# Optimization experiments

Hardware: AMD Instinct MI355X
Metric: run time of the kernel (lower is better)

The kernel has to match this reference:

```python
import jax, jax.numpy as jnp
import numpy as np

T_NO = 200
COS_NO = 24
HID_NO = 10


def make_cos_basis(t_no=T_NO, n=COS_NO, scale=6.0, shift=1.0):
    # [n, t_no] raised-cosine log-time basis, matching the torch loop
    phi = (jnp.pi / 2.0) * jnp.arange(n, dtype=jnp.float32)[:, None]
    x = jnp.arange(t_no, dtype=jnp.float32)[None, :]
    raw = scale * jnp.log(x + shift + 1e-7)
    b = 0.5 * jnp.cos(raw - phi) + 0.5
    keep = (raw >= phi - jnp.pi) & (raw <= phi + jnp.pi)
    return jnp.where(keep, b, 0.0)


def causal_basis_conv(syn, basis):
    # syn: [B, sub, T]; basis: [K, T_no]
    # out[b,s,k,t] = sum_d basis[k,d] * syn[b,s,t-d]   (causal conv)
    B, sub, T = syn.shape
    K, t_no = basis.shape
    w = jnp.flip(basis, axis=1)                    # cross-corr of flipped = conv
    kern = jnp.tile(w, (sub, 1))[:, None, :]       # [sub*K, 1, T_no]
    out = jax.lax.conv_general_dilated(
        syn, kern, window_strides=(1,), padding=[(t_no - 1, 0)],
        feature_group_count=sub,
        dimension_numbers=("NCH", "OIH", "NCH"))   # [B, sub*K, T]
    return out.reshape(B, sub, K, T)


def reference(S_e, S_i, temp, test, g_e, g_i, E_scale, I_scale,
              W_e_layer1, W_i_layer1, W_layer2, b_layer1,
              C_syn_e_raw, C_syn_i_raw, V_o):
    sub_no = C_syn_e_raw.shape[0]
    batch, T_data, _ = S_e.shape

    if test:  # inference branch (near-hard assignment via huge temperature)
        C_syn_e = jax.nn.softmax(C_syn_e_raw * 10000.0, axis=0)
        C_syn_i = jax.nn.softmax(C_syn_i_raw * 10000.0, axis=0)
    else:     # CustomSoftmax.forward == softmax(x * 1000, dim=0)
        C_syn_e = jax.nn.softmax((C_syn_e_raw + g_e) * 1000.0, axis=0)
        C_syn_i = jax.nn.softmax((C_syn_i_raw + g_i) * 1000.0, axis=0)

    # per-synapse scaling then synapse -> subunit grouping
    syn_e = jnp.einsum('bte,se->bst', S_e * jnp.exp(E_scale)[None, None, :], C_syn_e)
    syn_i = jnp.einsum('bti,si->bst', S_i * jnp.exp(I_scale)[None, None, :], C_syn_i)

    basis = make_cos_basis()                         # [24, T_no]
    Be = causal_basis_conv(syn_e, basis)             # [B, sub, 24, T]
    Bi = causal_basis_conv(syn_i, basis)

    We = W_e_layer1.reshape(sub_no, HID_NO, COS_NO)
    Wi = W_i_layer1.reshape(sub_no, HID_NO, COS_NO)
    # linear combination over basis == original per-channel kernels (linearity)
    pre = (jnp.einsum('bskt,shk->bsht', Be, We)
           + jnp.einsum('bskt,shk->bsht', Bi, Wi)
           + b_layer1.reshape(1, sub_no, HID_NO, 1))
    layer1_out = jnp.tanh(pre)                       # [B, sub, hid, T]

    # grouped 1x1 conv with exp(W_layer2): weighted sum over hid per subunit
    sub_out = jnp.einsum('bsht,sh->bts', layer1_out, jnp.exp(W_layer2))  # [B, T, sub]
    final = jnp.sum(sub_out, -1) + V_o               # [B, T]
    return (final, sub_out, C_syn_e, C_syn_i)


def setup_inputs() -> dict:
    key = jax.random.key(0)
    ks = jax.random.split(key, 8)
    batch, T_data = 4, 20000
    sub_no, E_no, I_no = 20, 2000, 500
    return {
        "S_e": jax.random.uniform(ks[0], (batch, T_data, E_no), jnp.float32),
        "S_i": jax.random.uniform(ks[1], (batch, T_data, I_no), jnp.float32),
        "temp": 1,
        "test": 1,
        "g_e": jax.random.normal(ks[2], (sub_no, E_no), jnp.float32),
        "g_i": jax.random.normal(ks[3], (sub_no, I_no), jnp.float32),
        "E_scale": jnp.zeros((E_no,), jnp.float32),
        "I_scale": jnp.zeros((I_no,), jnp.float32),
        "W_e_layer1": jax.random.normal(ks[4], (sub_no * HID_NO, COS_NO), jnp.float32) * 0.01,
        "W_i_layer1": jax.random.normal(ks[5], (sub_no * HID_NO, COS_NO), jnp.float32) * 0.01,
        "W_layer2": jnp.ones((sub_no, HID_NO), jnp.float32) * -1.0,
        "b_layer1": jnp.zeros((sub_no * HID_NO,), jnp.float32),
        "C_syn_e_raw": jax.random.normal(ks[6], (sub_no, E_no), jnp.float32) * 0.01,
        "C_syn_i_raw": jax.random.normal(ks[7], (sub_no, I_no), jnp.float32) * 0.01,
        "V_o": jnp.zeros((1,), jnp.float32),
    }
```

## Files before the change

### kernel.cpp

```cpp
#include <hip/hip_runtime.h>
#include <math.h>

#define B_   4
#define T_   20000
#define SUB  20
#define ENO  2000
#define INO  500
#define HID  10
#define NCOS 24
#define TNO  200

__global__ __launch_bounds__(256) void prep1_kernel(
    const float* __restrict__ Ce_raw, const float* __restrict__ Ci_raw,
    const float* __restrict__ ge, const float* __restrict__ gi,
    const float* __restrict__ Es, const float* __restrict__ Is,
    const float* __restrict__ W2, const int* __restrict__ testp,
    float* __restrict__ outCe, float* __restrict__ outCi,
    float* __restrict__ CwE, float* __restrict__ CwI, float* __restrict__ e2)
{
  int idx = blockIdx.x * 256 + threadIdx.x;
  int test = *testp;
  float scale = test ? 10000.f : 1000.f;
  if (idx < ENO + INO) {
    const float* raw; const float* g; float* outC; float* Cw; int n, col; float sc;
    if (idx < ENO) { raw = Ce_raw; g = ge; outC = outCe; Cw = CwE; n = ENO; col = idx;      sc = expf(Es[col]); }
    else           { raw = Ci_raw; g = gi; outC = outCi; Cw = CwI; n = INO; col = idx - ENO; sc = expf(Is[col]); }
    float v[SUB]; float m = -1e30f;
    #pragma unroll
    for (int s = 0; s < SUB; s++) {
      float x = raw[s * n + col];
      if (!test) x += g[s * n + col];
      x *= scale;
      v[s] = x; m = fmaxf(m, x);
    }
    float sum = 0.f;
    #pragma unroll
    for (int s = 0; s < SUB; s++) { v[s] = expf(v[s] - m); sum += v[s]; }
    float inv = 1.f / sum;
    #pragma unroll
    for (int s = 0; s < SUB; s++) { float c = v[s] * inv; outC[s * n + col] = c; Cw[s * n + col] = c * sc; }
  } else if (idx < ENO + INO + SUB * HID) {
    int j = idx - (ENO + INO);
    e2[j] = expf(W2[j]);
  }
}

__global__ __launch_bounds__(256) void prep2_kernel(
    const float* __restrict__ We, const float* __restrict__ Wi, float* __restrict__ Keff)
{
  int idx = blockIdx.x * 256 + threadIdx.x;
  if (idx >= 2 * SUB * HID * TNO) return;
  int d   = idx % TNO;
  int sh  = (idx / TNO) % (SUB * HID);
  int src = idx / (TNO * SUB * HID);
  const float* W = src ? Wi : We;
  const float PIF = 3.14159265358979323846f;
  float raw = 6.0f * logf((float)d + 1.0f + 1e-7f);
  float acc = 0.f;
  #pragma unroll
  for (int k = 0; k < NCOS; k++) {
    float ph = 1.57079632679489662f * (float)k;
    if (raw >= ph - PIF && raw <= ph + PIF) {
      acc += W[sh * NCOS + k] * (0.5f * cosf(raw - ph) + 0.5f);
    }
  }
  Keff[idx] = acc;
}

__global__ __launch_bounds__(256, 2) void gemm_syn_kernel(
    const float* __restrict__ S_e, const float* __restrict__ S_i,
    const float* __restrict__ CwE, const float* __restrict__ CwI,
    float* __restrict__ synE, float* __restrict__ synI)
{
  const int b  = blockIdx.y;
  const int t0 = blockIdx.x * 16;

  __shared__ __align__(16) float sS[16 * 528];
  __shared__ __align__(16) float sCw[20 * 512];

  const int tid = threadIdx.x;
  const int l   = tid & 63;
  const int w   = tid >> 6;
  const int s0  = w * 5;
  const int tg  = l & 1;
  const int ep  = l >> 1;

  if (tid < 192)            { int r = tid / 12, c = tid % 12;            sS[r * 528 + 500 + c] = 0.f; }
  else if (tid < 432)       { int u = tid - 192; int s = u / 12, c = u % 12; sCw[s * 512 + 500 + c] = 0.f; }

  float acc[8][5] = {};

  for (int z = 0; z < 5; z++) {
    const bool isE = (z < 4);
    {
      const float* __restrict__ src = isE ? (S_e + ((long)(b * T_ + t0)) * ENO + z * 500)
                                          : (S_i + ((long)(b * T_ + t0)) * INO);
      const int rs = isE ? ENO : INO;
      for (int u = tid; u < 2000; u += 256) {
        int r = u / 125, k = u - r * 125;
        float4 v = *(const float4*)&src[(long)r * rs + 4 * k];
        *(float4*)&sS[r * 528 + 4 * k] = v;
      }
      const float* __restrict__ csrc = isE ? (CwE + z * 500) : CwI;
      const int cs2 = isE ? ENO : INO;
      for (int u = tid; u < 2500; u += 256) {
        int s = u / 125, k = u - s * 125;
        float4 v = *(const float4*)&csrc[(long)s * cs2 + 4 * k];
        *(float4*)&sCw[s * 512 + 4 * k] = v;
      }
    }
    __syncthreads();

    #pragma unroll
    for (int step = 0; step < 4; step++) {
      const int e = 4 * ep + 128 * step;
      float4 cw[5];
      #pragma unroll
      for (int j = 0; j < 5; j++) cw[j] = *(float4*)&sCw[(s0 + j) * 512 + e];
      #pragma unroll
      for (int tt = 0; tt < 8; tt++) {
        float4 sv = *(float4*)&sS[(tg + 2 * tt) * 528 + e];
        #pragma unroll
        for (int j = 0; j < 5; j++) {
          acc[tt][j] += sv.x * cw[j].x;
          acc[tt][j] += sv.y * cw[j].y;
          acc[tt][j] += sv.z * cw[j].z;
          acc[tt][j] += sv.w * cw[j].w;
        }
      }
    }
    __syncthreads();

    if (z == 3 || z == 4) {
      #pragma unroll
      for (int mask = 2; mask <= 32; mask <<= 1) {
        #pragma unroll
        for (int tt = 0; tt < 8; tt++)
          #pragma unroll
          for (int j = 0; j < 5; j++)
            acc[tt][j] += __shfl_xor(acc[tt][j], mask, 64);
      }
      float* __restrict__ dst = (z == 3) ? synE : synI;
      if (l < 2) {
        #pragma unroll
        for (int j = 0; j < 5; j++)
          #pragma unroll
          for (int tt = 0; tt < 8; tt++)
            dst[((long)b * SUB + s0 + j) * T_ + t0 + tg + 2 * tt] = acc[tt][j];
      }
      #pragma unroll
      for (int tt = 0; tt < 8; tt++)
        #pragma unroll
        for (int j = 0; j < 5; j++) acc[tt][j] = 0.f;
    }
  }
}

__global__ __launch_bounds__(256, 2) void conv_kernel(
    const float* __restrict__ synE, const float* __restrict__ synI,
    const float* __restrict__ Keff, const float* __restrict__ e2,
    const float* __restrict__ b1, float* __restrict__ sub_bst)
{
  const int chunk = blockIdx.x;
  const int s = blockIdx.y;
  const int b = blockIdx.z;
  const int cs = chunk * 1000;

  __shared__ __align__(16) float se[1200];
  __shared__ __align__(16) float si[1200];
  __shared__ __align__(16) float te[HID * TNO];
  __shared__ __align__(16) float ti[HID * TNO];
  __shared__ float se2[HID], sb[HID];

  const int tid = threadIdx.x;
  const float* __restrict__ pe = &synE[((long)b * SUB + s) * T_];
  const float* __restrict__ pin = &synI[((long)b * SUB + s) * T_];

  for (int i4 = tid; i4 < 300; i4 += 256) {
    int gt = cs - 200 + i4 * 4;
    float4 ve = make_float4(0.f, 0.f, 0.f, 0.f);
    float4 vi = make_float4(0.f, 0.f, 0.f, 0.f);
    if (gt >= 0) { ve = *(const float4*)&pe[gt]; vi = *(const float4*)&pin[gt]; }
    *(float4*)&se[i4 * 4] = ve;
    *(float4*)&si[i4 * 4] = vi;
  }
  const float* __restrict__ ke = &Keff[(long)s * HID * TNO];
  const float* __restrict__ ki = &Keff[((long)SUB + s) * HID * TNO];
  for (int i4 = tid; i4 < 500; i4 += 256) {
    *(float4*)&te[i4 * 4] = *(const float4*)&ke[i4 * 4];
    *(float4*)&ti[i4 * 4] = *(const float4*)&ki[i4 * 4];
  }
  if (tid < HID) { se2[tid] = e2[s * HID + tid]; sb[tid] = b1[s * HID + tid]; }
  __syncthreads();

  if (tid >= 250) return;
  const int lofs = 200 + 4 * tid;
  float so[4] = {0.f, 0.f, 0.f, 0.f};

  #pragma unroll
  for (int half = 0; half < 2; half++) {
    const int h0 = half * 5;
    float acc[5][4] = {};
    float we[8], wi[8];
    *(float4*)&we[4] = *(float4*)&se[lofs];
    *(float4*)&wi[4] = *(float4*)&si[lofs];
    for (int dstep = 0; dstep < 50; dstep++) {
      const int d0 = dstep * 4;
      *(float4*)&we[0] = *(float4*)&se[lofs - d0 - 4];
      *(float4*)&wi[0] = *(float4*)&si[lofs - d0 - 4];
      float4 tpe[5], tpi[5];
      #pragma unroll
      for (int h = 0; h < 5; h++) {
        tpe[h] = *(float4*)&te[(h0 + h) * TNO + d0];
        tpi[h] = *(float4*)&ti[(h0 + h) * TNO + d0];
      }
      #pragma unroll
      for (int dd = 0; dd < 4; dd++) {
        #pragma unroll
        for (int h = 0; h < 5; h++) {
          float tapeh = ((float*)&tpe[h])[dd];
          float tapih = ((float*)&tpi[h])[dd];
          #pragma unroll
          for (int j = 0; j < 4; j++) {
            acc[h][j] += tapeh * we[4 + j - dd];
            acc[h][j] += tapih * wi[4 + j - dd];
          }
        }
      }
      #pragma unroll
      for (int m = 0; m < 4; m++) { we[4 + m] = we[m]; wi[4 + m] = wi[m]; }
    }
    #pragma unroll
    for (int h = 0; h < 5; h++) {
      float eh = se2[h0 + h], bh = sb[h0 + h];
      #pragma unroll
      for (int j = 0; j < 4; j++) so[j] += eh * tanhf(acc[h][j] + bh);
    }
  }
  int t0 = cs + 4 * tid;
  *(float4*)&sub_bst[((long)b * SUB + s) * T_ + t0] = *(float4*)&so[0];
}

__global__ __launch_bounds__(256) void final_kernel(
    const float* __restrict__ sub_bst, const float* __restrict__ Vo,
    float* __restrict__ out_final, float* __restrict__ out_sub)
{
  int t = blockIdx.x * 256 + threadIdx.x;
  int b = blockIdx.y;
  if (t >= T_) return;
  float vo = Vo[0];
  float sum = 0.f;
  #pragma unroll
  for (int s = 0; s < SUB; s++) {
    float v = sub_bst[((long)b * SUB + s) * T_ + t];
    sum += v;
    out_sub[(((long)b * T_) + t) * SUB + s] = v;
  }
  out_final[(long)b * T_ + t] = sum + vo;
}

extern "C" void kernel_launch(void* const* d_in, const int* in_sizes, int n_in,
                              void* d_out, int out_size, void* d_ws, size_t ws_size,
                              hipStream_t stream)
{
  const float* S_e    = (const float*)d_in[0];
  const float* S_i    = (const float*)d_in[1];
  const int*   testp  = (const int*)d_in[3];
  const float* g_e    = (const float*)d_in[4];
  const float* g_i    = (const float*)d_in[5];
  const float* Es     = (const float*)d_in[6];
  const float* Is     = (const float*)d_in[7];
  const float* We     = (const float*)d_in[8];
  const float* Wi     = (const float*)d_in[9];
  const float* W2     = (const float*)d_in[10];
  const float* b1     = (const float*)d_in[11];
  const float* Ce_raw = (const float*)d_in[12];
  const float* Ci_raw = (const float*)d_in[13];
  const float* Vo     = (const float*)d_in[14];

  float* ws   = (float*)d_ws;
  float* CwE  = ws;
  float* CwI  = ws + 40000;
  float* Keff = ws + 50000;
  float* e2   = ws + 130000;
  float* synE = ws + 130200;
  float* synI = synE + 1600000;
  float* subb = synI + 1600000;

  float* out     = (float*)d_out;
  float* o_final = out;
  float* o_sub   = out + 80000;
  float* o_Ce    = out + 1680000;
  float* o_Ci    = out + 1720000;

  prep1_kernel<<<11, 256, 0, stream>>>(Ce_raw, Ci_raw, g_e, g_i, Es, Is, W2, testp,
                                       o_Ce, o_Ci, CwE, CwI, e2);
  prep2_kernel<<<(2 * SUB * HID * TNO + 255) / 256, 256, 0, stream>>>(We, Wi, Keff);
  gemm_syn_kernel<<<dim3(T_ / 16, B_), 256, 0, stream>>>(S_e, S_i, CwE, CwI, synE, synI);
  conv_kernel<<<dim3(20, SUB, B_), 256, 0, stream>>>(synE, synI, Keff, e2, b1, subb);
  final_kernel<<<dim3((T_ + 255) / 256, B_), 256, 0, stream>>>(subb, Vo, o_final, o_sub);
}
```

Before: 740.0 us.

## Prefetch S tiles into registers and read padded Cw weights from global

```diff
diff --git a/kernel.cpp b/kernel.cpp
--- a/kernel.cpp
+++ b/kernel.cpp
@@ -16,15 +16,15 @@
     const float* __restrict__ Es, const float* __restrict__ Is,
     const float* __restrict__ W2, const int* __restrict__ testp,
     float* __restrict__ outCe, float* __restrict__ outCi,
-    float* __restrict__ CwE, float* __restrict__ CwI, float* __restrict__ e2)
+    float* __restrict__ CwPE, float* __restrict__ CwPI, float* __restrict__ e2)
 {
   int idx = blockIdx.x * 256 + threadIdx.x;
   int test = *testp;
   float scale = test ? 10000.f : 1000.f;
   if (idx < ENO + INO) {
-    const float* raw; const float* g; float* outC; float* Cw; int n, col; float sc;
-    if (idx < ENO) { raw = Ce_raw; g = ge; outC = outCe; Cw = CwE; n = ENO; col = idx;      sc = expf(Es[col]); }
-    else           { raw = Ci_raw; g = gi; outC = outCi; Cw = CwI; n = INO; col = idx - ENO; sc = expf(Is[col]); }
+    const float* raw; const float* g; float* outC; int n, col; float sc;
+    if (idx < ENO) { raw = Ce_raw; g = ge; outC = outCe; n = ENO; col = idx;       sc = expf(Es[col]); }
+    else           { raw = Ci_raw; g = gi; outC = outCi; n = INO; col = idx - ENO; sc = expf(Is[col]); }
     float v[SUB]; float m = -1e30f;
     #pragma unroll
     for (int s = 0; s < SUB; s++) {
@@ -37,11 +37,27 @@
     #pragma unroll
     for (int s = 0; s < SUB; s++) { v[s] = expf(v[s] - m); sum += v[s]; }
     float inv = 1.f / sum;
-    #pragma unroll
-    for (int s = 0; s < SUB; s++) { float c = v[s] * inv; outC[s * n + col] = c; Cw[s * n + col] = c * sc; }
+    if (idx < ENO) {
+      int z = col / 500, e2c = col - z * 500;
+      #pragma unroll
+      for (int s = 0; s < SUB; s++) {
+        float c = v[s] * inv; outC[s * n + col] = c;
+        CwPE[((long)(z * SUB + s)) * 512 + e2c] = c * sc;
+      }
+    } else {
+      #pragma unroll
+      for (int s = 0; s < SUB; s++) {
+        float c = v[s] * inv; outC[s * n + col] = c;
+        CwPI[(long)s * 512 + col] = c * sc;
+      }
+    }
   } else if (idx < ENO + INO + SUB * HID) {
     int j = idx - (ENO + INO);
     e2[j] = expf(W2[j]);
+  } else if (idx < ENO + INO + SUB * HID + 960 + 240) {
+    int j = idx - (ENO + INO + SUB * HID);
+    if (j < 960) { int z = j / 240, s = (j / 12) % SUB, c = j % 12; CwPE[((long)(z * SUB + s)) * 512 + 500 + c] = 0.f; }
+    else         { int j2 = j - 960; int s = j2 / 12, c = j2 % 12;  CwPI[(long)s * 512 + 500 + c] = 0.f; }
   }
 }
 
@@ -67,59 +83,65 @@
   Keff[idx] = acc;
 }
 
-__global__ __launch_bounds__(256, 2) void gemm_syn_kernel(
+__global__ __launch_bounds__(256, 4) void gemm_syn_kernel(
     const float* __restrict__ S_e, const float* __restrict__ S_i,
-    const float* __restrict__ CwE, const float* __restrict__ CwI,
+    const float* __restrict__ CwPE, const float* __restrict__ CwPI,
     float* __restrict__ synE, float* __restrict__ synI)
 {
   const int b  = blockIdx.y;
   const int t0 = blockIdx.x * 16;
-
   __shared__ __align__(16) float sS[16 * 528];
-  __shared__ __align__(16) float sCw[20 * 512];
 
   const int tid = threadIdx.x;
   const int l   = tid & 63;
   const int w   = tid >> 6;
   const int s0  = w * 5;
-  const int tg  = l & 1;
-  const int ep  = l >> 1;
-
-  if (tid < 192)            { int r = tid / 12, c = tid % 12;            sS[r * 528 + 500 + c] = 0.f; }
-  else if (tid < 432)       { int u = tid - 192; int s = u / 12, c = u % 12; sCw[s * 512 + 500 + c] = 0.f; }
-
-  float acc[8][5] = {};
+  const int rp  = l & 3;
+  const int ep  = l >> 2;
+
+  if (tid < 192) { int r = tid / 12, c = tid % 12; sS[r * 528 + 500 + c] = 0.f; }
+
+  float acc[4][5] = {};
+  float4 pS[8];
+
+  const long rowE = ((long)b * T_ + t0) * ENO;
+  const long rowI = ((long)b * T_ + t0) * INO;
+
+  #pragma unroll
+  for (int p = 0; p < 8; p++) {
+    int u = tid + 256 * p;
+    if (u < 2000) { int r = u / 125, k = u - r * 125; pS[p] = *(const float4*)&S_e[rowE + (long)r * ENO + 4 * k]; }
+  }
 
   for (int z = 0; z < 5; z++) {
     const bool isE = (z < 4);
-    {
-      const float* __restrict__ src = isE ? (S_e + ((long)(b * T_ + t0)) * ENO + z * 500)
-                                          : (S_i + ((long)(b * T_ + t0)) * INO);
-      const int rs = isE ? ENO : INO;
-      for (int u = tid; u < 2000; u += 256) {
-        int r = u / 125, k = u - r * 125;
-        float4 v = *(const float4*)&src[(long)r * rs + 4 * k];
-        *(float4*)&sS[r * 528 + 4 * k] = v;
-      }
-      const float* __restrict__ csrc = isE ? (CwE + z * 500) : CwI;
-      const int cs2 = isE ? ENO : INO;
-      for (int u = tid; u < 2500; u += 256) {
-        int s = u / 125, k = u - s * 125;
-        float4 v = *(const float4*)&csrc[(long)s * cs2 + 4 * k];
-        *(float4*)&sCw[s * 512 + 4 * k] = v;
+    #pragma unroll
+    for (int p = 0; p < 8; p++) {
+      int u = tid + 256 * p;
+      if (u < 2000) { int r = u / 125, k = u - r * 125; *(float4*)&sS[r * 528 + 4 * k] = pS[p]; }
+    }
+    if (z < 4) {
+      const bool nE = (z + 1 < 4);
+      const float* __restrict__ src = nE ? (S_e + rowE + (z + 1) * 500) : (S_i + rowI);
+      const int rs = nE ? ENO : INO;
+      #pragma unroll
+      for (int p = 0; p < 8; p++) {
+        int u = tid + 256 * p;
+        if (u < 2000) { int r = u / 125, k = u - r * 125; pS[p] = *(const float4*)&src[(long)r * rs + 4 * k]; }
       }
     }
     __syncthreads();
 
-    #pragma unroll
-    for (int step = 0; step < 4; step++) {
-      const int e = 4 * ep + 128 * step;
+    const float* __restrict__ cwb = isE ? (CwPE + ((long)z * SUB) * 512) : CwPI;
+    #pragma unroll
+    for (int step = 0; step < 8; step++) {
+      const int e = 4 * ep + 64 * step;
       float4 cw[5];
       #pragma unroll
-      for (int j = 0; j < 5; j++) cw[j] = *(float4*)&sCw[(s0 + j) * 512 + e];
-      #pragma unroll
-      for (int tt = 0; tt < 8; tt++) {
-        float4 sv = *(float4*)&sS[(tg + 2 * tt) * 528 + e];
+      for (int j = 0; j < 5; j++) cw[j] = *(const float4*)&cwb[(s0 + j) * 512 + e];
+      #pragma unroll
+      for (int tt = 0; tt < 4; tt++) {
+        float4 sv = *(float4*)&sS[(rp + 4 * tt) * 528 + e];
         #pragma unroll
         for (int j = 0; j < 5; j++) {
           acc[tt][j] += sv.x * cw[j].x;
@@ -129,30 +151,29 @@
         }
       }
     }
-    __syncthreads();
-
-    if (z == 3 || z == 4) {
-      #pragma unroll
-      for (int mask = 2; mask <= 32; mask <<= 1) {
-        #pragma unroll
-        for (int tt = 0; tt < 8; tt++)
+
+    if (z >= 3) {
+      #pragma unroll
+      for (int mask = 4; mask <= 32; mask <<= 1)
+        #pragma unroll
+        for (int tt = 0; tt < 4; tt++)
           #pragma unroll
           for (int j = 0; j < 5; j++)
             acc[tt][j] += __shfl_xor(acc[tt][j], mask, 64);
-      }
       float* __restrict__ dst = (z == 3) ? synE : synI;
-      if (l < 2) {
+      if (l < 4) {
         #pragma unroll
         for (int j = 0; j < 5; j++)
           #pragma unroll
-          for (int tt = 0; tt < 8; tt++)
-            dst[((long)b * SUB + s0 + j) * T_ + t0 + tg + 2 * tt] = acc[tt][j];
-      }
-      #pragma unroll
-      for (int tt = 0; tt < 8; tt++)
+          for (int tt = 0; tt < 4; tt++)
+            dst[((long)b * SUB + s0 + j) * T_ + t0 + rp + 4 * tt] = acc[tt][j];
+      }
+      #pragma unroll
+      for (int tt = 0; tt < 4; tt++)
         #pragma unroll
         for (int j = 0; j < 5; j++) acc[tt][j] = 0.f;
     }
+    __syncthreads();
   }
 }
 
@@ -279,11 +300,11 @@
   const float* Vo     = (const float*)d_in[14];
 
   float* ws   = (float*)d_ws;
-  float* CwE  = ws;
-  float* CwI  = ws + 40000;
-  float* Keff = ws + 50000;
-  float* e2   = ws + 130000;
-  float* synE = ws + 130200;
+  float* CwPE = ws;
+  float* CwPI = ws + 40960;
+  float* Keff = ws + 51200;
+  float* e2   = ws + 131200;
+  float* synE = ws + 131400;
   float* synI = synE + 1600000;
   float* subb = synI + 1600000;
 
@@ -293,10 +314,10 @@
   float* o_Ce    = out + 1680000;
   float* o_Ci    = out + 1720000;
 
-  prep1_kernel<<<11, 256, 0, stream>>>(Ce_raw, Ci_raw, g_e, g_i, Es, Is, W2, testp,
-                                       o_Ce, o_Ci, CwE, CwI, e2);
+  prep1_kernel<<<16, 256, 0, stream>>>(Ce_raw, Ci_raw, g_e, g_i, Es, Is, W2, testp,
+                                       o_Ce, o_Ci, CwPE, CwPI, e2);
   prep2_kernel<<<(2 * SUB * HID * TNO + 255) / 256, 256, 0, stream>>>(We, Wi, Keff);
-  gemm_syn_kernel<<<dim3(T_ / 16, B_), 256, 0, stream>>>(S_e, S_i, CwE, CwI, synE, synI);
+  gemm_syn_kernel<<<dim3(T_ / 16, B_), 256, 0, stream>>>(S_e, S_i, CwPE, CwPI, synE, synI);
   conv_kernel<<<dim3(20, SUB, B_), 256, 0, stream>>>(synE, synI, Keff, e2, b1, subb);
   final_kernel<<<dim3((T_ + 255) / 256, B_), 256, 0, stream>>>(subb, Vo, o_final, o_sub);
 }
```

Measured after the change: 1.077 ms. 1.46x slower.
